# Kernel optimization log

Measured on AMD Instinct MI355X. Metric: run time of the kernel, lower is better.

Reference implementation:

```python
import jax, jax.numpy as jnp
import numpy as np

TEMPERATURE = 8.0  # sqrt(d_k)
WINDOW = 2
GATE_THRESH = 0.5
NEG_INF = -1e30


def setup_inputs() -> dict:
    key = jax.random.key(0)
    k1, k2, k3, k4 = jax.random.split(key, 4)
    BH, L, D = 32, 2048, 64
    return {
        "q": jax.random.normal(k1, (BH, L, D), dtype=jnp.float32),
        "k": jax.random.normal(k2, (BH, L, D), dtype=jnp.float32),
        "v": jax.random.normal(k3, (BH, L, D), dtype=jnp.float32),
        "gate_w": jax.random.normal(k4, (1, D), dtype=jnp.float32) * 0.1,
        "gate_b": jnp.zeros((1,), dtype=jnp.float32),
    }


def reference(q, k, v, gate_w, gate_b):
    # q,k: [BH, L, D]; v: [BH, L, Dv]
    BH, Lq, D = q.shape
    Lk = k.shape[1]
    attn = jnp.einsum("bqd,bkd->bqk", q, k) / TEMPERATURE  # [BH, Lq, Lk]
    # per-query gate: if sigmoid(linear(q)) <= thresh, restrict to sliding window
    gate = jax.nn.sigmoid(jnp.einsum("bqd,od->bqo", q, gate_w) + gate_b) > GATE_THRESH  # [BH,Lq,1]
    i = jnp.arange(Lq)[:, None]
    j = jnp.arange(Lk)[None, :]
    window_ok = jnp.abs(i - j) <= WINDOW  # [Lq, Lk]; equals left=max(0,i-W), right=min(Lk,i+W+1)
    allowed = gate | window_ok[None, :, :]  # gate True -> full attention
    attn = jnp.where(allowed, attn, NEG_INF)
    attn = jax.nn.softmax(attn, axis=2)
    # dropout omitted (eval mode)
    out = jnp.einsum("bqk,bkd->bqd", attn, v)
    return out, attn
```

## Files before the change

kernel.cpp:

```cpp
#include <hip/hip_runtime.h>


typedef short bf16x8 __attribute__((ext_vector_type(8)));
typedef float f32x4  __attribute__((ext_vector_type(4)));

#define LSEQ 2048
#define DDIM 64
#define KB_STRIDE 72
#define VT_STRIDE 36
#define PB_STRIDE 36

__device__ __forceinline__ unsigned short f2bf(float x) {
    unsigned int u = __float_as_uint(x);
    u += 0x7FFFu + ((u >> 16) & 1u);
    return (unsigned short)(u >> 16);
}

__global__ __launch_bounds__(256)
void dsa_attn_kernel(const float* __restrict__ Q,
                     const float* __restrict__ K,
                     const float* __restrict__ V,
                     const float* __restrict__ GW,
                     const float* __restrict__ GB,
                     float* __restrict__ OUT,
                     float* __restrict__ ATT)
{
    __shared__ unsigned short Kbuf[32 * KB_STRIDE];
    __shared__ unsigned short Vt[64 * VT_STRIDE];
    __shared__ float Pbuf[4][16 * PB_STRIDE];
    __shared__ float gateF[64];

    const int bx   = blockIdx.x;
    const int bh   = bx >> 5;
    const int q0   = (bx & 31) << 6;
    const int tid  = threadIdx.x;
    const int wave = tid >> 6;
    const int lane = tid & 63;
    const int m16  = lane & 15;
    const int quad = lane >> 4;

    const float* qb = Q + ((size_t)bh * LSEQ + q0) * DDIM;
    const float* kb = K + (size_t)bh * LSEQ * DDIM;
    const float* vb = V + (size_t)bh * LSEQ * DDIM;

    if (tid < 64) {
        const float* qr = qb + tid * DDIM;
        float a = 0.f;
        #pragma unroll 8
        for (int d = 0; d < DDIM; ++d) a += qr[d] * GW[d];
        a += GB[0];
        gateF[tid] = (a > 0.f) ? 1.f : 0.f;
    }

    bf16x8 qfrag[2];
    {
        const float* qr = qb + ((wave << 4) + m16) * DDIM + (quad << 3);
        #pragma unroll
        for (int db = 0; db < 2; ++db) {
            const float* p = qr + db * 32;
            bf16x8 f;
            #pragma unroll
            for (int j = 0; j < 8; ++j) f[j] = (short)f2bf(p[j]);
            qfrag[db] = f;
        }
    }

    __syncthreads();
    float gate[4];
    int   irow[4];
    #pragma unroll
    for (int r = 0; r < 4; ++r) {
        gate[r] = gateF[(wave << 4) + (quad << 2) + r];
        irow[r] = q0 + (wave << 4) + (quad << 2) + r;
    }

    float lsum[4] = {0.f, 0.f, 0.f, 0.f};
    for (int kt = 0; kt < LSEQ / 32; ++kt) {
        __syncthreads();
        {
            const int e   = tid << 3;
            const int key = e >> 6;
            const int d   = e & 63;
            const float* src = kb + (size_t)(kt * 32 + key) * DDIM + d;
            unsigned short* dst = &Kbuf[key * KB_STRIDE + d];
            #pragma unroll
            for (int j = 0; j < 8; ++j) dst[j] = f2bf(src[j]);
        }
        __syncthreads();
        #pragma unroll
        for (int nt = 0; nt < 2; ++nt) {
            const unsigned short* kr = &Kbuf[(nt * 16 + m16) * KB_STRIDE + (quad << 3)];
            bf16x8 kf0 = *(const bf16x8*)(kr);
            bf16x8 kf1 = *(const bf16x8*)(kr + 32);
            f32x4 acc = {0.f, 0.f, 0.f, 0.f};
            acc = __builtin_amdgcn_mfma_f32_16x16x32_bf16(qfrag[0], kf0, acc, 0, 0, 0);
            acc = __builtin_amdgcn_mfma_f32_16x16x32_bf16(qfrag[1], kf1, acc, 0, 0, 0);
            const int jcol = kt * 32 + nt * 16 + m16;
            #pragma unroll
            for (int r = 0; r < 4; ++r) {
                int dist = irow[r] - jcol; if (dist < 0) dist = -dist;
                const bool allowed = (gate[r] > 0.5f) || (dist <= 2);
                const float s = acc[r] * 0.125f;
                lsum[r] += allowed ? __expf(s) : 0.f;
            }
        }
    }
    #pragma unroll
    for (int r = 0; r < 4; ++r) {
        float x = lsum[r];
        x += __shfl_xor(x, 1);
        x += __shfl_xor(x, 2);
        x += __shfl_xor(x, 4);
        x += __shfl_xor(x, 8);
        lsum[r] = 1.0f / x;
    }

    f32x4 oacc[4];
    #pragma unroll
    for (int dt = 0; dt < 4; ++dt) oacc[dt] = (f32x4){0.f, 0.f, 0.f, 0.f};

    for (int kt = 0; kt < LSEQ / 32; ++kt) {
        __syncthreads();
        {
            const int e   = tid << 3;
            const int key = e >> 6;
            const int d   = e & 63;
            const float* src = kb + (size_t)(kt * 32 + key) * DDIM + d;
            unsigned short* dst = &Kbuf[key * KB_STRIDE + d];
            #pragma unroll
            for (int j = 0; j < 8; ++j) dst[j] = f2bf(src[j]);
        }
        {
            const int key = tid & 31;
            const int db  = (tid >> 5) << 3;
            const float* src = vb + (size_t)(kt * 32 + key) * DDIM + db;
            #pragma unroll
            for (int j = 0; j < 8; ++j)
                Vt[(db + j) * VT_STRIDE + key] = f2bf(src[j]);
        }
        __syncthreads();

        #pragma unroll
        for (int nt = 0; nt < 2; ++nt) {
            const unsigned short* kr = &Kbuf[(nt * 16 + m16) * KB_STRIDE + (quad << 3)];
            bf16x8 kf0 = *(const bf16x8*)(kr);
            bf16x8 kf1 = *(const bf16x8*)(kr + 32);
            f32x4 acc = {0.f, 0.f, 0.f, 0.f};
            acc = __builtin_amdgcn_mfma_f32_16x16x32_bf16(qfrag[0], kf0, acc, 0, 0, 0);
            acc = __builtin_amdgcn_mfma_f32_16x16x32_bf16(qfrag[1], kf1, acc, 0, 0, 0);
            const int jcol = kt * 32 + nt * 16 + m16;
            #pragma unroll
            for (int r = 0; r < 4; ++r) {
                int dist = irow[r] - jcol; if (dist < 0) dist = -dist;
                const bool allowed = (gate[r] > 0.5f) || (dist <= 2);
                const float s = acc[r] * 0.125f;
                const float p = allowed ? __expf(s) * lsum[r] : 0.f;
                Pbuf[wave][((quad << 2) + r) * PB_STRIDE + nt * 16 + m16] = p;
            }
        }
        __syncthreads();

        const float* pr = &Pbuf[wave][m16 * PB_STRIDE + (quad << 3)];
        f32x4 p0 = *(const f32x4*)(pr);
        f32x4 p1 = *(const f32x4*)(pr + 4);
        float* ap = ATT + ((size_t)bh * LSEQ + q0 + (wave << 4) + m16) * LSEQ
                        + kt * 32 + (quad << 3);
        *(f32x4*)(ap)     = p0;
        *(f32x4*)(ap + 4) = p1;

        bf16x8 pf;
        #pragma unroll
        for (int j = 0; j < 4; ++j) {
            pf[j]     = (short)f2bf(p0[j]);
            pf[4 + j] = (short)f2bf(p1[j]);
        }
        #pragma unroll
        for (int dt = 0; dt < 4; ++dt) {
            const unsigned short* vr = &Vt[(dt * 16 + m16) * VT_STRIDE + (quad << 3)];
            ushort4 va  = *(const ushort4*)(vr);
            ushort4 vb4 = *(const ushort4*)(vr + 4);
            bf16x8 vf;
            vf[0] = (short)va.x;  vf[1] = (short)va.y;
            vf[2] = (short)va.z;  vf[3] = (short)va.w;
            vf[4] = (short)vb4.x; vf[5] = (short)vb4.y;
            vf[6] = (short)vb4.z; vf[7] = (short)vb4.w;
            oacc[dt] = __builtin_amdgcn_mfma_f32_16x16x32_bf16(pf, vf, oacc[dt], 0, 0, 0);
        }
    }

    float* ob = OUT + ((size_t)bh * LSEQ + q0 + (wave << 4)) * DDIM;
    #pragma unroll
    for (int dt = 0; dt < 4; ++dt) {
        #pragma unroll
        for (int r = 0; r < 4; ++r) {
            ob[((quad << 2) + r) * DDIM + dt * 16 + m16] = oacc[dt][r];
        }
    }
}

extern "C" void kernel_launch(void* const* d_in, const int* in_sizes, int n_in,
                              void* d_out, int out_size, void* d_ws, size_t ws_size,
                              hipStream_t stream) {
    const float* q  = (const float*)d_in[0];
    const float* k  = (const float*)d_in[1];
    const float* v  = (const float*)d_in[2];
    const float* gw = (const float*)d_in[3];
    const float* gb = (const float*)d_in[4];

    float* out  = (float*)d_out;
    float* attn = out + (size_t)32 * 2048 * 64;

    dim3 grid(32 * (2048 / 64));
    dim3 block(256);
    dsa_attn_kernel<<<grid, block, 0, stream>>>(q, k, v, gw, gb, out, attn);
}
```

Before: 772.9 us.

## Split gated rows from windowed rows and precompute bf16 K and transposed V

A prep kernel converts K to bf16 and V to a transposed bf16 layout in workspace once, so the main kernel reads fragments straight from global memory instead of converting into shared memory on every tile. In the main kernel, the query rows of each block are compacted by gate value with a ballot. Only the gated rows run full-length MFMA attention. Non-gated rows compute a 5-key windowed softmax with wave reductions and write a mostly-zero attention row. This skips dense work for roughly half the rows but adds an extra launch, global-load latency with no LDS reuse, and load imbalance between waves.

```diff
diff --git a/kernel.cpp b/kernel.cpp
--- a/kernel.cpp
+++ b/kernel.cpp
@@ -6,8 +6,6 @@
 
 #define LSEQ 2048
 #define DDIM 64
-#define KB_STRIDE 72
-#define VT_STRIDE 36
 #define PB_STRIDE 36
 
 __device__ __forceinline__ unsigned short f2bf(float x) {
@@ -16,19 +14,83 @@
     return (unsigned short)(u >> 16);
 }
 
+__device__ __forceinline__ unsigned int pk2f(float a, float b) {
+    return (unsigned int)f2bf(a) | ((unsigned int)f2bf(b) << 16);
+}
+
+__device__ __forceinline__ unsigned int pk2u(unsigned short a, unsigned short b) {
+    return (unsigned int)a | ((unsigned int)b << 16);
+}
+
+__device__ __forceinline__ float pick5(int jj, float e0, float e1, float e2,
+                                       float e3, float e4) {
+    float r = 0.f;
+    r = (jj == 0) ? e0 : r;
+    r = (jj == 1) ? e1 : r;
+    r = (jj == 2) ? e2 : r;
+    r = (jj == 3) ? e3 : r;
+    r = (jj == 4) ? e4 : r;
+    return r;
+}
+
 __global__ __launch_bounds__(256)
-void dsa_attn_kernel(const float* __restrict__ Q,
-                     const float* __restrict__ K,
-                     const float* __restrict__ V,
-                     const float* __restrict__ GW,
-                     const float* __restrict__ GB,
-                     float* __restrict__ OUT,
-                     float* __restrict__ ATT)
+void dsa_prep(const float* __restrict__ K, const float* __restrict__ V,
+              unsigned short* __restrict__ Kb, unsigned short* __restrict__ Vt)
 {
-    __shared__ unsigned short Kbuf[32 * KB_STRIDE];
-    __shared__ unsigned short Vt[64 * VT_STRIDE];
+    const int bh  = blockIdx.x >> 5;
+    const int k0  = (blockIdx.x & 31) << 6;
+    const int tid = threadIdx.x;
+    __shared__ unsigned short tileT[64][73];
+
+    const int key = tid >> 2;
+    const int d0  = (tid & 3) << 4;
+    const float* srcK = K + ((size_t)bh * LSEQ + k0 + key) * DDIM + d0;
+    const float* srcV = V + ((size_t)bh * LSEQ + k0 + key) * DDIM + d0;
+    {
+        uint4 w0, w1;
+        w0.x = pk2f(srcK[0],  srcK[1]);  w0.y = pk2f(srcK[2],  srcK[3]);
+        w0.z = pk2f(srcK[4],  srcK[5]);  w0.w = pk2f(srcK[6],  srcK[7]);
+        w1.x = pk2f(srcK[8],  srcK[9]);  w1.y = pk2f(srcK[10], srcK[11]);
+        w1.z = pk2f(srcK[12], srcK[13]); w1.w = pk2f(srcK[14], srcK[15]);
+        unsigned short* dst = Kb + ((size_t)bh * LSEQ + k0 + key) * DDIM + d0;
+        *(uint4*)(dst)     = w0;
+        *(uint4*)(dst + 8) = w1;
+    }
+    #pragma unroll
+    for (int j = 0; j < 16; ++j) tileT[d0 + j][key] = f2bf(srcV[j]);
+    __syncthreads();
+    {
+        const int d   = tid >> 2;
+        const int kk0 = (tid & 3) << 4;
+        uint4 w0, w1;
+        w0.x = pk2u(tileT[d][kk0 + 0],  tileT[d][kk0 + 1]);
+        w0.y = pk2u(tileT[d][kk0 + 2],  tileT[d][kk0 + 3]);
+        w0.z = pk2u(tileT[d][kk0 + 4],  tileT[d][kk0 + 5]);
+        w0.w = pk2u(tileT[d][kk0 + 6],  tileT[d][kk0 + 7]);
+        w1.x = pk2u(tileT[d][kk0 + 8],  tileT[d][kk0 + 9]);
+        w1.y = pk2u(tileT[d][kk0 + 10], tileT[d][kk0 + 11]);
+        w1.z = pk2u(tileT[d][kk0 + 12], tileT[d][kk0 + 13]);
+        w1.w = pk2u(tileT[d][kk0 + 14], tileT[d][kk0 + 15]);
+        unsigned short* dst = Vt + (size_t)bh * DDIM * LSEQ + (size_t)d * LSEQ + k0 + kk0;
+        *(uint4*)(dst)     = w0;
+        *(uint4*)(dst + 8) = w1;
+    }
+}
+
+__global__ __launch_bounds__(256, 4)
+void dsa_main(const float* __restrict__ Q,
+              const unsigned short* __restrict__ Kb,
+              const unsigned short* __restrict__ Vt,
+              const float* __restrict__ K32,
+              const float* __restrict__ V32,
+              const float* __restrict__ GW,
+              const float* __restrict__ GB,
+              float* __restrict__ OUT,
+              float* __restrict__ ATT)
+{
     __shared__ float Pbuf[4][16 * PB_STRIDE];
-    __shared__ float gateF[64];
+    __shared__ int   sidx[64];
+    __shared__ int   gShared;
 
     const int bx   = blockIdx.x;
     const int bh   = bx >> 5;
@@ -40,160 +102,191 @@
     const int quad = lane >> 4;
 
     const float* qb = Q + ((size_t)bh * LSEQ + q0) * DDIM;
-    const float* kb = K + (size_t)bh * LSEQ * DDIM;
-    const float* vb = V + (size_t)bh * LSEQ * DDIM;
-
-    if (tid < 64) {
-        const float* qr = qb + tid * DDIM;
+
+    if (wave == 0) {
+        const float* qr = qb + lane * DDIM;
         float a = 0.f;
         #pragma unroll 8
         for (int d = 0; d < DDIM; ++d) a += qr[d] * GW[d];
         a += GB[0];
-        gateF[tid] = (a > 0.f) ? 1.f : 0.f;
-    }
-
-    bf16x8 qfrag[2];
-    {
-        const float* qr = qb + ((wave << 4) + m16) * DDIM + (quad << 3);
-        #pragma unroll
-        for (int db = 0; db < 2; ++db) {
-            const float* p = qr + db * 32;
-            bf16x8 f;
-            #pragma unroll
-            for (int j = 0; j < 8; ++j) f[j] = (short)f2bf(p[j]);
-            qfrag[db] = f;
-        }
-    }
-
+        const bool gt = (a > 0.f);
+        const unsigned long long b = __ballot(gt);
+        const int below = __popcll(b & ((1ull << lane) - 1ull));
+        const int g     = __popcll(b);
+        const int pos   = gt ? below : (g + (lane - below));
+        sidx[pos] = lane;
+        if (lane == 0) gShared = g;
+    }
     __syncthreads();
-    float gate[4];
-    int   irow[4];
-    #pragma unroll
-    for (int r = 0; r < 4; ++r) {
-        gate[r] = gateF[(wave << 4) + (quad << 2) + r];
-        irow[r] = q0 + (wave << 4) + (quad << 2) + r;
-    }
-
-    float lsum[4] = {0.f, 0.f, 0.f, 0.f};
-    for (int kt = 0; kt < LSEQ / 32; ++kt) {
-        __syncthreads();
+    const int g = gShared;
+    const int T = (g + 15) >> 4;
+
+    if (wave < T) {
+        const unsigned short* kbb = Kb + (size_t)bh * LSEQ * DDIM;
+        const unsigned short* vtb = Vt + (size_t)bh * DDIM * LSEQ;
+        const int  myIdx = (wave << 4) + m16;
+        const bool valid = myIdx < g;
+        const int  srow  = sidx[valid ? myIdx : (g - 1)];
+
+        bf16x8 qfrag[2];
         {
-            const int e   = tid << 3;
-            const int key = e >> 6;
-            const int d   = e & 63;
-            const float* src = kb + (size_t)(kt * 32 + key) * DDIM + d;
-            unsigned short* dst = &Kbuf[key * KB_STRIDE + d];
-            #pragma unroll
-            for (int j = 0; j < 8; ++j) dst[j] = f2bf(src[j]);
-        }
-        __syncthreads();
-        #pragma unroll
-        for (int nt = 0; nt < 2; ++nt) {
-            const unsigned short* kr = &Kbuf[(nt * 16 + m16) * KB_STRIDE + (quad << 3)];
-            bf16x8 kf0 = *(const bf16x8*)(kr);
-            bf16x8 kf1 = *(const bf16x8*)(kr + 32);
-            f32x4 acc = {0.f, 0.f, 0.f, 0.f};
-            acc = __builtin_amdgcn_mfma_f32_16x16x32_bf16(qfrag[0], kf0, acc, 0, 0, 0);
-            acc = __builtin_amdgcn_mfma_f32_16x16x32_bf16(qfrag[1], kf1, acc, 0, 0, 0);
-            const int jcol = kt * 32 + nt * 16 + m16;
-            #pragma unroll
-            for (int r = 0; r < 4; ++r) {
-                int dist = irow[r] - jcol; if (dist < 0) dist = -dist;
-                const bool allowed = (gate[r] > 0.5f) || (dist <= 2);
-                const float s = acc[r] * 0.125f;
-                lsum[r] += allowed ? __expf(s) : 0.f;
-            }
-        }
-    }
-    #pragma unroll
-    for (int r = 0; r < 4; ++r) {
-        float x = lsum[r];
-        x += __shfl_xor(x, 1);
-        x += __shfl_xor(x, 2);
-        x += __shfl_xor(x, 4);
-        x += __shfl_xor(x, 8);
-        lsum[r] = 1.0f / x;
-    }
-
-    f32x4 oacc[4];
-    #pragma unroll
-    for (int dt = 0; dt < 4; ++dt) oacc[dt] = (f32x4){0.f, 0.f, 0.f, 0.f};
-
-    for (int kt = 0; kt < LSEQ / 32; ++kt) {
-        __syncthreads();
-        {
-            const int e   = tid << 3;
-            const int key = e >> 6;
-            const int d   = e & 63;
-            const float* src = kb + (size_t)(kt * 32 + key) * DDIM + d;
-            unsigned short* dst = &Kbuf[key * KB_STRIDE + d];
-            #pragma unroll
-            for (int j = 0; j < 8; ++j) dst[j] = f2bf(src[j]);
-        }
-        {
-            const int key = tid & 31;
-            const int db  = (tid >> 5) << 3;
-            const float* src = vb + (size_t)(kt * 32 + key) * DDIM + db;
-            #pragma unroll
-            for (int j = 0; j < 8; ++j)
-                Vt[(db + j) * VT_STRIDE + key] = f2bf(src[j]);
-        }
-        __syncthreads();
-
-        #pragma unroll
-        for (int nt = 0; nt < 2; ++nt) {
-            const unsigned short* kr = &Kbuf[(nt * 16 + m16) * KB_STRIDE + (quad << 3)];
-            bf16x8 kf0 = *(const bf16x8*)(kr);
-            bf16x8 kf1 = *(const bf16x8*)(kr + 32);
-            f32x4 acc = {0.f, 0.f, 0.f, 0.f};
-            acc = __builtin_amdgcn_mfma_f32_16x16x32_bf16(qfrag[0], kf0, acc, 0, 0, 0);
-            acc = __builtin_amdgcn_mfma_f32_16x16x32_bf16(qfrag[1], kf1, acc, 0, 0, 0);
-            const int jcol = kt * 32 + nt * 16 + m16;
-            #pragma unroll
-            for (int r = 0; r < 4; ++r) {
-                int dist = irow[r] - jcol; if (dist < 0) dist = -dist;
-                const bool allowed = (gate[r] > 0.5f) || (dist <= 2);
-                const float s = acc[r] * 0.125f;
-                const float p = allowed ? __expf(s) * lsum[r] : 0.f;
-                Pbuf[wave][((quad << 2) + r) * PB_STRIDE + nt * 16 + m16] = p;
-            }
-        }
-        __syncthreads();
-
-        const float* pr = &Pbuf[wave][m16 * PB_STRIDE + (quad << 3)];
-        f32x4 p0 = *(const f32x4*)(pr);
-        f32x4 p1 = *(const f32x4*)(pr + 4);
-        float* ap = ATT + ((size_t)bh * LSEQ + q0 + (wave << 4) + m16) * LSEQ
-                        + kt * 32 + (quad << 3);
-        *(f32x4*)(ap)     = p0;
-        *(f32x4*)(ap + 4) = p1;
-
-        bf16x8 pf;
-        #pragma unroll
-        for (int j = 0; j < 4; ++j) {
-            pf[j]     = (short)f2bf(p0[j]);
-            pf[4 + j] = (short)f2bf(p1[j]);
-        }
-        #pragma unroll
-        for (int dt = 0; dt < 4; ++dt) {
-            const unsigned short* vr = &Vt[(dt * 16 + m16) * VT_STRIDE + (quad << 3)];
-            ushort4 va  = *(const ushort4*)(vr);
-            ushort4 vb4 = *(const ushort4*)(vr + 4);
-            bf16x8 vf;
-            vf[0] = (short)va.x;  vf[1] = (short)va.y;
-            vf[2] = (short)va.z;  vf[3] = (short)va.w;
-            vf[4] = (short)vb4.x; vf[5] = (short)vb4.y;
-            vf[6] = (short)vb4.z; vf[7] = (short)vb4.w;
-            oacc[dt] = __builtin_amdgcn_mfma_f32_16x16x32_bf16(pf, vf, oacc[dt], 0, 0, 0);
-        }
-    }
-
-    float* ob = OUT + ((size_t)bh * LSEQ + q0 + (wave << 4)) * DDIM;
-    #pragma unroll
-    for (int dt = 0; dt < 4; ++dt) {
+            const float* qr = qb + srow * DDIM + (quad << 3);
+            #pragma unroll
+            for (int db = 0; db < 2; ++db) {
+                const float* p = qr + db * 32;
+                bf16x8 f;
+                #pragma unroll
+                for (int j = 0; j < 8; ++j) f[j] = (short)f2bf(p[j]);
+                qfrag[db] = f;
+            }
+        }
+
+        const unsigned short* kp0 = kbb + (size_t)m16 * DDIM + (quad << 3);
+
+        float lsum[4] = {0.f, 0.f, 0.f, 0.f};
+        bf16x8 c0 = *(const bf16x8*)(kp0);
+        bf16x8 c1 = *(const bf16x8*)(kp0 + 32);
+        bf16x8 c2 = *(const bf16x8*)(kp0 + 16 * DDIM);
+        bf16x8 c3 = *(const bf16x8*)(kp0 + 16 * DDIM + 32);
+        for (int kt = 0; kt < 64; ++kt) {
+            const unsigned short* np = kp0 + (size_t)(((kt + 1) & 63) * 32) * DDIM;
+            bf16x8 n0 = *(const bf16x8*)(np);
+            bf16x8 n1 = *(const bf16x8*)(np + 32);
+            bf16x8 n2 = *(const bf16x8*)(np + 16 * DDIM);
+            bf16x8 n3 = *(const bf16x8*)(np + 16 * DDIM + 32);
+            f32x4 a0 = {0.f, 0.f, 0.f, 0.f}, a1 = {0.f, 0.f, 0.f, 0.f};
+            a0 = __builtin_amdgcn_mfma_f32_16x16x32_bf16(qfrag[0], c0, a0, 0, 0, 0);
+            a0 = __builtin_amdgcn_mfma_f32_16x16x32_bf16(qfrag[1], c1, a0, 0, 0, 0);
+            a1 = __builtin_amdgcn_mfma_f32_16x16x32_bf16(qfrag[0], c2, a1, 0, 0, 0);
+            a1 = __builtin_amdgcn_mfma_f32_16x16x32_bf16(qfrag[1], c3, a1, 0, 0, 0);
+            #pragma unroll
+            for (int r = 0; r < 4; ++r)
+                lsum[r] += __expf(a0[r] * 0.125f) + __expf(a1[r] * 0.125f);
+            c0 = n0; c1 = n1; c2 = n2; c3 = n3;
+        }
+        float inv[4];
         #pragma unroll
         for (int r = 0; r < 4; ++r) {
-            ob[((quad << 2) + r) * DDIM + dt * 16 + m16] = oacc[dt][r];
+            float x = lsum[r];
+            x += __shfl_xor(x, 1); x += __shfl_xor(x, 2);
+            x += __shfl_xor(x, 4); x += __shfl_xor(x, 8);
+            inv[r] = 1.0f / x;
+        }
+
+        f32x4 oacc[4];
+        #pragma unroll
+        for (int dt = 0; dt < 4; ++dt) oacc[dt] = (f32x4){0.f, 0.f, 0.f, 0.f};
+        float* pw  = &Pbuf[wave][0];
+        float* ap0 = ATT + ((size_t)(bh * LSEQ + q0 + srow)) * LSEQ + (quad << 3);
+        const unsigned short* vp0 = vtb + (size_t)m16 * LSEQ + (quad << 3);
+
+        for (int kt = 0; kt < 64; ++kt) {
+            const unsigned short* kp = kp0 + (size_t)(kt * 32) * DDIM;
+            bf16x8 k0 = *(const bf16x8*)(kp);
+            bf16x8 k1 = *(const bf16x8*)(kp + 32);
+            bf16x8 k2 = *(const bf16x8*)(kp + 16 * DDIM);
+            bf16x8 k3 = *(const bf16x8*)(kp + 16 * DDIM + 32);
+            const unsigned short* vp = vp0 + kt * 32;
+            bf16x8 v0 = *(const bf16x8*)(vp);
+            bf16x8 v1 = *(const bf16x8*)(vp + 16 * LSEQ);
+            bf16x8 v2 = *(const bf16x8*)(vp + 32 * LSEQ);
+            bf16x8 v3 = *(const bf16x8*)(vp + 48 * LSEQ);
+
+            f32x4 a0 = {0.f, 0.f, 0.f, 0.f}, a1 = {0.f, 0.f, 0.f, 0.f};
+            a0 = __builtin_amdgcn_mfma_f32_16x16x32_bf16(qfrag[0], k0, a0, 0, 0, 0);
+            a0 = __builtin_amdgcn_mfma_f32_16x16x32_bf16(qfrag[1], k1, a0, 0, 0, 0);
+            a1 = __builtin_amdgcn_mfma_f32_16x16x32_bf16(qfrag[0], k2, a1, 0, 0, 0);
+            a1 = __builtin_amdgcn_mfma_f32_16x16x32_bf16(qfrag[1], k3, a1, 0, 0, 0);
+
+            #pragma unroll
+            for (int r = 0; r < 4; ++r) {
+                const int prow = (quad << 2) + r;
+                pw[prow * PB_STRIDE + m16]      = __expf(a0[r] * 0.125f) * inv[r];
+                pw[prow * PB_STRIDE + 16 + m16] = __expf(a1[r] * 0.125f) * inv[r];
+            }
+            const float* prd = pw + m16 * PB_STRIDE + (quad << 3);
+            f32x4 p0 = *(const f32x4*)(prd);
+            f32x4 p1 = *(const f32x4*)(prd + 4);
+            if (valid) {
+                float* ap = ap0 + kt * 32;
+                *(f32x4*)(ap)     = p0;
+                *(f32x4*)(ap + 4) = p1;
+            }
+            bf16x8 pf;
+            #pragma unroll
+            for (int j = 0; j < 4; ++j) {
+                pf[j]     = (short)f2bf(p0[j]);
+                pf[4 + j] = (short)f2bf(p1[j]);
+            }
+            oacc[0] = __builtin_amdgcn_mfma_f32_16x16x32_bf16(pf, v0, oacc[0], 0, 0, 0);
+            oacc[1] = __builtin_amdgcn_mfma_f32_16x16x32_bf16(pf, v1, oacc[1], 0, 0, 0);
+            oacc[2] = __builtin_amdgcn_mfma_f32_16x16x32_bf16(pf, v2, oacc[2], 0, 0, 0);
+            oacc[3] = __builtin_amdgcn_mfma_f32_16x16x32_bf16(pf, v3, oacc[3], 0, 0, 0);
+        }
+        #pragma unroll
+        for (int r = 0; r < 4; ++r) {
+            const int idx = (wave << 4) + (quad << 2) + r;
+            if (idx < g) {
+                const int orow = sidx[idx];
+                float* ob = OUT + ((size_t)(bh * LSEQ + q0 + orow)) * DDIM + m16;
+                ob[0]  = oacc[0][r];
+                ob[16] = oacc[1][r];
+                ob[32] = oacc[2][r];
+                ob[48] = oacc[3][r];
+            }
+        }
+    }
+
+    const int nw    = 64 - g;
+    const int nww   = (T < 4) ? (4 - T) : 4;
+    const int wslot = (T < 4) ? (wave - T) : wave;
+    if (wslot >= 0 && nw > 0) {
+        for (int ii = wslot; ii < nw; ii += nww) {
+            const int row = sidx[g + ii];
+            const int i   = q0 + row;
+            const float qd = qb[row * DDIM + lane];
+
+            float e[5];
+            float denom = 0.f;
+            #pragma unroll
+            for (int jj = 0; jj < 5; ++jj) {
+                const int  j  = i - 2 + jj;
+                const bool ok = (j >= 0) && (j < LSEQ);
+                const int  jc = ok ? j : 0;
+                float t = qd * K32[((size_t)bh * LSEQ + jc) * DDIM + lane];
+                t += __shfl_xor(t, 1);  t += __shfl_xor(t, 2);
+                t += __shfl_xor(t, 4);  t += __shfl_xor(t, 8);
+                t += __shfl_xor(t, 16); t += __shfl_xor(t, 32);
+                const float ee = ok ? __expf(t * 0.125f) : 0.f;
+                e[jj] = ee;
+                denom += ee;
+            }
+            const float invd = 1.f / denom;
+            #pragma unroll
+            for (int jj = 0; jj < 5; ++jj) e[jj] *= invd;
+
+            float o = 0.f;
+            #pragma unroll
+            for (int jj = 0; jj < 5; ++jj) {
+                const int  j  = i - 2 + jj;
+                const int  jc = (j >= 0 && j < LSEQ) ? j : 0;
+                o += e[jj] * V32[((size_t)bh * LSEQ + jc) * DDIM + lane];
+            }
+            OUT[((size_t)(bh * LSEQ + i)) * DDIM + lane] = o;
+
+            float* ar = ATT + ((size_t)(bh * LSEQ + i)) * LSEQ;
+            const int jlo = i - 2;
+            #pragma unroll
+            for (int it = 0; it < 8; ++it) {
+                const int c = (it << 8) + (lane << 2);
+                f32x4 z = {0.f, 0.f, 0.f, 0.f};
+                if (c + 3 >= jlo && c <= jlo + 4) {
+                    #pragma unroll
+                    for (int t4 = 0; t4 < 4; ++t4)
+                        z[t4] = pick5(c + t4 - jlo, e[0], e[1], e[2], e[3], e[4]);
+                }
+                *(f32x4*)(ar + c) = z;
+            }
         }
     }
 }
@@ -210,7 +303,10 @@
     float* out  = (float*)d_out;
     float* attn = out + (size_t)32 * 2048 * 64;
 
-    dim3 grid(32 * (2048 / 64));
+    unsigned short* Kb = (unsigned short*)d_ws;
+    unsigned short* Vt = Kb + (size_t)32 * 2048 * 64;
+
     dim3 block(256);
-    dsa_attn_kernel<<<grid, block, 0, stream>>>(q, k, v, gw, gb, out, attn);
-}
+    dsa_prep<<<dim3(32 * 32), block, 0, stream>>>(k, v, Kb, Vt);
+    dsa_main<<<dim3(32 * 32), block, 0, stream>>>(q, Kb, Vt, k, v, gw, gb, out, attn);
+}
```

Result: slower. 792.3 us (+2.5%).
